# Performance work log

Measured on AMD Instinct MI355X. Metric: run time of the kernel, lower is better.

The kernel has to match this reference:

```python
import jax, jax.numpy as jnp
from jax import lax
import numpy as np

SHAPE = (50, 60, 65)   # -> after net: (17, 27, 32), flatten = 14688
NEG = 0.01             # LeakyReLU default slope
B, N = 8, 80000        # batch size, total active voxels


def _lrelu(x):
    return jnp.where(x >= 0, x, NEG * x)


def _sparse_conv(x, w, b, m):
    # Regular (non-submanifold) sparse conv == dense VALID conv on densified
    # input (inactive sites are 0 so they contribute nothing). Output site is
    # active iff any input site in the kernel footprint is active; bias is
    # added only at active output sites.
    k = w.shape[2]
    y = lax.conv_general_dilated(x, w, (1, 1, 1), 'VALID',
                                 dimension_numbers=('NCDHW', 'OIDHW', 'NCDHW'))
    m2 = lax.reduce_window(m, 0.0, lax.max, (1, 1, k, k, k), (1, 1, 1, 1, 1), 'VALID')
    y = jnp.where(m2 > 0, y + b[None, :, None, None, None], 0.0)
    return y, m2


def _sparse_maxpool(x, m, k):
    # spconv SparseMaxPool: max over ACTIVE sites only (inactive excluded, not 0)
    xm = jnp.where(m > 0, x, -jnp.inf)
    p = lax.reduce_window(xm, -jnp.inf, lax.max, (1, 1, k, k, k), (1, 1, 1, 1, 1), 'VALID')
    m2 = lax.reduce_window(m, 0.0, lax.max, (1, 1, k, k, k), (1, 1, 1, 1, 1), 'VALID')
    return jnp.where(m2 > 0, p, 0.0), m2


def setup_inputs() -> dict:
    key = jax.random.key(0)
    ks = jax.random.split(key, 24)
    D, H, W = SHAPE
    features = jax.random.normal(ks[0], (N, 1), dtype=jnp.float32)
    bi = jax.random.randint(ks[1], (N,), 0, B)
    zi = jax.random.randint(ks[2], (N,), 0, D)
    yi = jax.random.randint(ks[3], (N,), 0, H)
    xi = jax.random.randint(ks[4], (N,), 0, W)
    coors = jnp.stack([bi, zi, yi, xi], axis=1).astype(jnp.int32)
    s = 0.05
    p = {}
    p['w1'] = jax.random.normal(ks[5], (32, 1, 4, 4, 4), jnp.float32) * s
    p['b1'] = jax.random.normal(ks[6], (32,), jnp.float32) * s
    p['w2'] = jax.random.normal(ks[7], (32, 32, 4, 4, 4), jnp.float32) * s
    p['b2'] = jax.random.normal(ks[8], (32,), jnp.float32) * s
    p['w3'] = jax.random.normal(ks[9], (32, 32, 4, 4, 4), jnp.float32) * s
    p['b3'] = jax.random.normal(ks[10], (32,), jnp.float32) * s
    p['w4'] = jax.random.normal(ks[11], (32, 32, 4, 4, 4), jnp.float32) * s
    p['b4'] = jax.random.normal(ks[12], (32,), jnp.float32) * s
    p['w5'] = jax.random.normal(ks[13], (32, 32, 4, 4, 4), jnp.float32) * s
    p['b5'] = jax.random.normal(ks[14], (32,), jnp.float32) * s
    p['w6'] = jax.random.normal(ks[15], (32, 32, 4, 4, 4), jnp.float32) * s
    p['b6'] = jax.random.normal(ks[16], (32,), jnp.float32) * s
    p['w7'] = jax.random.normal(ks[17], (1, 32, 4, 4, 4), jnp.float32) * s
    p['b7'] = jax.random.normal(ks[18], (1,), jnp.float32) * s
    p['W8'] = jax.random.normal(ks[19], (14688, 1000), jnp.float32) * 0.01
    p['b8'] = jax.random.normal(ks[20], (1000,), jnp.float32) * s
    p['W9'] = jax.random.normal(ks[21], (1000, 1000), jnp.float32) * 0.03
    p['b9'] = jax.random.normal(ks[22], (1000,), jnp.float32) * s
    p['W10'] = jax.random.normal(ks[23], (1000, 1), jnp.float32) * 0.03
    p['b10'] = jnp.zeros((1,), jnp.float32)
    return dict(features=features, coors=coors, batch_size=B, **p)


def reference(features, coors, batch_size,
              w1, b1, w2, b2, w3, b3, w4, b4, w5, b5, w6, b6, w7, b7,
              W8, b8, W9, b9, W10, b10):
    D, H, W = SHAPE
    bi, zi, yi, xi = coors[:, 0], coors[:, 1], coors[:, 2], coors[:, 3]
    dense = jnp.zeros((batch_size, 1, D, H, W), features.dtype)
    dense = dense.at[bi, 0, zi, yi, xi].set(features[:, 0])
    mask = jnp.zeros((batch_size, 1, D, H, W), features.dtype)
    mask = mask.at[bi, 0, zi, yi, xi].set(1.0)

    x, m = _sparse_conv(dense, w1, b1, mask); x = _lrelu(x)
    x, m = _sparse_conv(x, w2, b2, m);        x = _lrelu(x)
    x, m = _sparse_maxpool(x, m, 5)
    x, m = _sparse_conv(x, w3, b3, m);        x = _lrelu(x)
    x, m = _sparse_conv(x, w4, b4, m);        x = _lrelu(x)
    x, m = _sparse_maxpool(x, m, 5)
    x, m = _sparse_conv(x, w5, b5, m);        x = _lrelu(x)
    x, m = _sparse_conv(x, w6, b6, m);        x = _lrelu(x)
    x, m = _sparse_conv(x, w7, b7, m);        x = _lrelu(x)
    x, m = _sparse_maxpool(x, m, 5)

    # ToDense (inactive sites already 0) + Flatten -> [B, 14688]
    h = x.reshape(x.shape[0], -1)
    h = _lrelu(h @ W8 + b8)
    h = _lrelu(h @ W9 + b9)
    out = _lrelu(h @ W10 + b10)
    return out
```

## Files before the change

### kernel.cpp

```cpp
#include <hip/hip_runtime.h>
#include <cstddef>


#define NEGSLOPE 0.01f
#define NINF (-3.0e38f)

#define TZ 4
#define TY 4
#define TXT 16
#define IZ 7
#define IY 7
#define IX 19
#define NV (IZ*IY*IX)

typedef __attribute__((ext_vector_type(8)))  short    short8;
typedef __attribute__((ext_vector_type(4)))  unsigned uint4v;
typedef __attribute__((ext_vector_type(16))) float    floatx16;

constexpr int ilog2c(int v) { return v == 1 ? 0 : 1 + ilog2c(v / 2); }

__device__ __forceinline__ float lrelu(float v) { return v >= 0.f ? v : NEGSLOPE * v; }

__device__ __forceinline__ unsigned short f2bf(float f) {
  unsigned b = __float_as_uint(f);
  return (unsigned short)((b + 0x7fffu + ((b >> 16) & 1u)) >> 16);
}
__device__ __forceinline__ float bf2f(unsigned short h) {
  return __uint_as_float(((unsigned)h) << 16);
}
__device__ __forceinline__ unsigned splitpair(float a, float b, unsigned& lo) {
  unsigned short ha = f2bf(a), hb = f2bf(b);
  unsigned short la = f2bf(a - bf2f(ha)), lb = f2bf(b - bf2f(hb));
  lo = (unsigned)la | ((unsigned)lb << 16);
  return (unsigned)ha | ((unsigned)hb << 16);
}

__device__ __forceinline__ short8 ld_frag(const uint2* s2, int v, int oct) {
  uint2 u0 = s2[v * 5 + oct * 2];
  uint2 u1 = s2[v * 5 + oct * 2 + 1];
  uint4v t; t.x = u0.x; t.y = u0.y; t.z = u1.x; t.w = u1.y;
  return __builtin_bit_cast(short8, t);
}

__global__ void k_claim(const int* __restrict__ coors, unsigned* __restrict__ claim, int N) {
  int i = blockIdx.x * blockDim.x + threadIdx.x;
  if (i >= N) return;
  int b = coors[4*i], z = coors[4*i+1], y = coors[4*i+2], x = coors[4*i+3];
  int v = ((b*50 + z)*60 + y)*65 + x;
  atomicMax(&claim[v], (unsigned)(i + 1));
}

__global__ void k_scatter(const int* __restrict__ coors, const float* __restrict__ feat,
                          const unsigned* __restrict__ claim,
                          float* __restrict__ x0, float* __restrict__ m0, int N) {
  int i = blockIdx.x * blockDim.x + threadIdx.x;
  if (i >= N) return;
  int b = coors[4*i], z = coors[4*i+1], y = coors[4*i+2], x = coors[4*i+3];
  int v = ((b*50 + z)*60 + y)*65 + x;
  m0[v] = 1.f;
  if (claim[v] == (unsigned)(i + 1)) x0[v] = feat[i];
}

__global__ void k_repack(const float* __restrict__ w, float* __restrict__ wr, int CI, int CO) {
  int i = blockIdx.x * blockDim.x + threadIdx.x;
  int tot = CO * CI * 64;
  if (i >= tot) return;
  int k = i & 63;
  int ci = (i >> 6) % CI;
  int co = i / (64 * CI);
  wr[(k * CI + ci) * CO + co] = w[i];
}

__global__ void k_repack_mfma(const float* __restrict__ w, unsigned short* __restrict__ tbl) {
  int i = blockIdx.x * blockDim.x + threadIdx.x;
  if (i >= 64*4*2*64) return;
  int lane = i & 63; int t = i >> 6;
  int pack = t & 1; t >>= 1;
  int pass = t & 3; int tap = t >> 2;
  int co = lane & 31; int oct = lane >> 5;
#pragma unroll
  for (int j = 0; j < 8; ++j) {
    int k = oct * 8 + j;
    int ci = pass * 8 + (k & 7);
    int part = ((k >> 3) ^ pack) & 1;
    float wv = w[((co * 32 + ci) << 6) + tap];
    unsigned short wh = f2bf(wv);
    unsigned short r = part ? f2bf(wv - bf2f(wh)) : wh;
    tbl[(size_t)i * 8 + j] = r;
  }
}

__global__ void kd_z(const float* __restrict__ in, float* __restrict__ o,
                     int Zi, int Yi, int Xi, int Zo, int K, int nI) {
  int gid = blockIdx.x * blockDim.x + threadIdx.x;
  int perOut = Zo * Yi * Xi;
  if (gid >= nI * perOut) return;
  int item = gid / perOut;
  int r = gid - item * perOut;
  int x = r % Xi; int t = r / Xi;
  int y = t % Yi; int z = t / Yi;
  const float* ib = in + (size_t)item * Zi * Yi * Xi;
  float mx = 0.f;
  for (int d = 0; d < K; d++) mx = fmaxf(mx, ib[((z + d) * Yi + y) * Xi + x]);
  o[gid] = mx;
}

__global__ void kd_y(const float* __restrict__ in, float* __restrict__ o,
                     int Zo, int Yi, int Xi, int Yo, int K, int nI) {
  int gid = blockIdx.x * blockDim.x + threadIdx.x;
  int perOut = Zo * Yo * Xi;
  if (gid >= nI * perOut) return;
  int item = gid / perOut;
  int r = gid - item * perOut;
  int x = r % Xi; int t = r / Xi;
  int y = t % Yo; int z = t / Yo;
  const float* ib = in + (size_t)item * Zo * Yi * Xi;
  float mx = 0.f;
  for (int d = 0; d < K; d++) mx = fmaxf(mx, ib[(z * Yi + y + d) * Xi + x]);
  o[gid] = mx;
}

__global__ void kd_x(const float* __restrict__ in, float* __restrict__ o,
                     int Zo, int Yo, int Xi, int Xo, int K, int nI) {
  int gid = blockIdx.x * blockDim.x + threadIdx.x;
  int perOut = Zo * Yo * Xo;
  if (gid >= nI * perOut) return;
  int item = gid / perOut;
  int r = gid - item * perOut;
  int x = r % Xo; int t = r / Xo;
  int y = t % Yo; int z = t / Yo;
  const float* ib = in + (size_t)item * Zo * Yo * Xi;
  float mx = 0.f;
  for (int d = 0; d < K; d++) mx = fmaxf(mx, ib[(z * Yo + y) * Xi + x + d]);
  o[gid] = mx;
}

template<int TZL, int TYL, int TXL, int IZL, int IYL, int IXL>
__global__ __launch_bounds__(256, 4)
void k_conv32m(const float* __restrict__ in, const unsigned short* __restrict__ tbl,
               const float* __restrict__ bias, const float* __restrict__ mo,
               float* __restrict__ out,
               int Zi, int Yi, int Xi, int Zo, int Yo, int Xo,
               int tilesZ, int tilesY, int tilesX) {
  constexpr int NVL = IZL * IYL * IXL;
  constexpr int LXs = ilog2c(TXL);
  constexpr int LYs = ilog2c(TYL);
  __shared__ unsigned sU[NVL * 10];
  const int perIn = Zi * Yi * Xi;
  const int perOut = Zo * Yo * Xo;
  int bid = blockIdx.x;
  int txi = bid % tilesX; bid /= tilesX;
  int tyi = bid % tilesY; bid /= tilesY;
  int tzi = bid % tilesZ; int item = bid / tilesZ;
  const int z0 = tzi * TZL, y0 = tyi * TYL, x0 = txi * TXL;
  const int tid = threadIdx.x;
  const int lane = tid & 63;
  const int col = lane & 31;
  const int oct = lane >> 5;
  const int wv  = tid >> 6;

  int lvBase0, lvBase1;
  {
    int vt0 = (2*wv + 0)*32 + col;
    int vt1 = (2*wv + 1)*32 + col;
    lvBase0 = ((vt0 >> (LXs+LYs))*IYL + ((vt0 >> LXs) & (TYL-1)))*IXL + (vt0 & (TXL-1));
    lvBase1 = ((vt1 >> (LXs+LYs))*IYL + ((vt1 >> LXs) & (TYL-1)))*IXL + (vt1 & (TXL-1));
  }

  floatx16 acc0, acc1;
#pragma unroll
  for (int r = 0; r < 16; ++r) { acc0[r] = 0.f; acc1[r] = 0.f; }

  const float* inb = in + (size_t)item * perIn * 32;
  const char* tb = (const char*)tbl + lane * 16;
  uint2* s2 = (uint2*)sU;

#pragma unroll 1
  for (int p = 0; p < 4; ++p) {
    __syncthreads();
    for (int idx = tid; idx < NVL; idx += 256) {
      int iz = idx / (IYL * IXL); int r = idx - iz * (IYL * IXL);
      int iy = r / IXL; int ix = r - iy * IXL;
      int gz = z0 + iz, gy = y0 + iy, gx = x0 + ix;
      float4 f0 = make_float4(0.f,0.f,0.f,0.f), f1 = make_float4(0.f,0.f,0.f,0.f);
      if (gz < Zi && gy < Yi && gx < Xi) {
        const float* vp = inb + (size_t)((gz * Yi + gy) * Xi + gx) * 32 + p * 8;
        f0 = *(const float4*)vp;
        f1 = *(const float4*)(vp + 4);
      }
      unsigned l0, l1, l2, l3;
      unsigned h0 = splitpair(f0.x, f0.y, l0);
      unsigned h1 = splitpair(f0.z, f0.w, l1);
      unsigned h2 = splitpair(f1.x, f1.y, l2);
      unsigned h3 = splitpair(f1.z, f1.w, l3);
      s2[idx * 5 + 0] = make_uint2(h0, h1);
      s2[idx * 5 + 1] = make_uint2(h2, h3);
      s2[idx * 5 + 2] = make_uint2(l0, l1);
      s2[idx * 5 + 3] = make_uint2(l2, l3);
    }
    __syncthreads();

    const char* tp = tb + (size_t)p * 2048;
#pragma unroll 2
    for (int tap = 0; tap < 64; ++tap) {
      int kz = tap >> 4, ky = (tap >> 2) & 3, kx = tap & 3;
      int sOff = (kz * IYL + ky) * IXL + kx;
      short8 b0 = *(const short8*)(tp + (size_t)tap * 8192);
      short8 b1 = *(const short8*)(tp + (size_t)tap * 8192 + 1024);
      short8 a0 = ld_frag(s2, lvBase0 + sOff, oct);
      short8 a1 = ld_frag(s2, lvBase1 + sOff, oct);
      acc0 = __builtin_amdgcn_mfma_f32_32x32x16_bf16(a0, b0, acc0, 0, 0, 0);
      acc0 = __builtin_amdgcn_mfma_f32_32x32x16_bf16(a0, b1, acc0, 0, 0, 0);
      acc1 = __builtin_amdgcn_mfma_f32_32x32x16_bf16(a1, b0, acc1, 0, 0, 0);
      acc1 = __builtin_amdgcn_mfma_f32_32x32x16_bf16(a1, b1, acc1, 0, 0, 0);
    }
  }

  const float bco = bias[col];
#pragma unroll
  for (int gg = 0; gg < 2; ++gg) {
    int vtb = (2*wv + gg) * 32;
#pragma unroll
    for (int rg = 0; rg < 16; ++rg) {
      int row = (rg & 3) + 8 * (rg >> 2) + 4 * oct;
      int vt = vtb + row;
      int oz = vt >> (LXs+LYs), oy = (vt >> LXs) & (TYL-1), ox = vt & (TXL-1);
      int gz = z0 + oz, gy = y0 + oy, gx = x0 + ox;
      if (gz < Zo && gy < Yo && gx < Xo) {
        int ov = item * perOut + (gz * Yo + gy) * Xo + gx;
        float val = (gg == 0) ? acc0[rg] : acc1[rg];
        bool act = mo[ov] > 0.f;
        out[(size_t)ov * 32 + col] = lrelu(act ? (val + bco) : 0.f);
      }
    }
  }
}

template<int TZL, int TYL, int TXL, int IZL, int IYL, int IXL>
static void launch_conv32(hipStream_t stream,
                          const float* in, const unsigned short* tbl, const float* bias,
                          const float* mo, float* o,
                          int Zi, int Yi, int Xi, int Zo, int Yo, int Xo, int nI) {
  int tz = (Zo + TZL - 1) / TZL, ty = (Yo + TYL - 1) / TYL, tx = (Xo + TXL - 1) / TXL;
  k_conv32m<TZL,TYL,TXL,IZL,IYL,IXL><<<nI * tz * ty * tx, 256, 0, stream>>>(
      in, tbl, bias, mo, o, Zi, Yi, Xi, Zo, Yo, Xo, tz, ty, tx);
}

__global__ __launch_bounds__(256, 2)
void k_conv1t(const float* __restrict__ in, const float* __restrict__ wr,
              const float* __restrict__ bias, const float* __restrict__ mo,
              float* __restrict__ out,
              int Zi, int Yi, int Xi, int Zo, int Yo, int Xo,
              int tilesZ, int tilesY, int tilesX) {
  __shared__ float sinf[NV];
  __shared__ float4 wsh[512];
  {
    const float4* wr4 = (const float4*)wr;
    for (int idx = threadIdx.x; idx < 512; idx += 256) wsh[idx] = wr4[idx];
  }
  const int perIn = Zi * Yi * Xi;
  const int perOut = Zo * Yo * Xo;
  int bid = blockIdx.x;
  int txi = bid % tilesX; bid /= tilesX;
  int tyi = bid % tilesY; bid /= tilesY;
  int tzi = bid % tilesZ; int item = bid / tilesZ;
  const int z0 = tzi * TZ, y0 = tyi * TY, x0 = txi * TXT;
  const int tid = threadIdx.x;
  const int ox = tid & 15, oy = (tid >> 4) & 3, oz = tid >> 6;

  const float* inb = in + (size_t)item * perIn;
  for (int idx = tid; idx < NV; idx += 256) {
    int iz = idx / (IY * IX); int r = idx - iz * (IY * IX);
    int iy = r / IX; int ix = r - iy * IX;
    int gz = z0 + iz, gy = y0 + iy, gx = x0 + ix;
    float val = 0.f;
    if (gz < Zi && gy < Yi && gx < Xi)
      val = inb[(size_t)((gz * Yi + gy) * Xi + gx)];
    sinf[idx] = val;
  }
  __syncthreads();

  float4 acc[8];
#pragma unroll
  for (int j = 0; j < 8; ++j) acc[j] = make_float4(0.f, 0.f, 0.f, 0.f);

#pragma unroll 1
  for (int tap = 0; tap < 64; ++tap) {
    int kz = tap >> 4, ky = (tap >> 2) & 3, kx = tap & 3;
    int lv = ((oz + kz) * IY + (oy + ky)) * IX + (ox + kx);
    float av = sinf[lv];
#pragma unroll
    for (int j = 0; j < 8; ++j) {
      float4 wvv = wsh[tap * 8 + j];
      acc[j].x = fmaf(av, wvv.x, acc[j].x);
      acc[j].y = fmaf(av, wvv.y, acc[j].y);
      acc[j].z = fmaf(av, wvv.z, acc[j].z);
      acc[j].w = fmaf(av, wvv.w, acc[j].w);
    }
  }

  int gz = z0 + oz, gy = y0 + oy, gx = x0 + ox;
  if (gz < Zo && gy < Yo && gx < Xo) {
    int ov = item * perOut + (gz * Yo + gy) * Xo + gx;
    bool act = mo[ov] > 0.f;
    const float4* b4 = (const float4*)bias;
    float* op = out + (size_t)ov * 32;
#pragma unroll
    for (int j = 0; j < 8; ++j) {
      float4 r = acc[j]; float4 bj = b4[j];
      r.x = lrelu(act ? (r.x + bj.x) : 0.f);
      r.y = lrelu(act ? (r.y + bj.y) : 0.f);
      r.z = lrelu(act ? (r.z + bj.z) : 0.f);
      r.w = lrelu(act ? (r.w + bj.w) : 0.f);
      *(float4*)(op + j * 4) = r;
    }
  }
}

__global__ __launch_bounds__(256, 2)
void k_conv7t(const float* __restrict__ in, const float* __restrict__ wr,
              const float* __restrict__ bias, const float* __restrict__ mo,
              float* __restrict__ out,
              int Zi, int Yi, int Xi, int Zo, int Yo, int Xo,
              int tilesZ, int tilesY, int tilesX) {
  __shared__ float4 sin4[4][NV];
  __shared__ float4 wsh[512];
  {
    const float4* wr4 = (const float4*)wr;
    for (int idx = threadIdx.x; idx < 512; idx += 256) wsh[idx] = wr4[idx];
  }
  const int perIn = Zi * Yi * Xi;
  const int perOut = Zo * Yo * Xo;
  int bid = blockIdx.x;
  int txi = bid % tilesX; bid /= tilesX;
  int tyi = bid % tilesY; bid /= tilesY;
  int tzi = bid % tilesZ; int item = bid / tilesZ;
  const int z0 = tzi * TZ, y0 = tyi * TY, x0 = txi * TXT;
  const int tid = threadIdx.x;
  const int ox = tid & 15, oy = (tid >> 4) & 3, oz = tid >> 6;

  const float* inb = in + (size_t)item * perIn * 32;
  float acc = 0.f;

#pragma unroll 1
  for (int h = 0; h < 2; ++h) {
    __syncthreads();
    for (int idx = tid; idx < NV * 4; idx += 256) {
      int q = idx / NV; int v = idx - q * NV;
      int iz = v / (IY * IX); int r = v - iz * (IY * IX);
      int iy = r / IX; int ix = r - iy * IX;
      int gz = z0 + iz, gy = y0 + iy, gx = x0 + ix;
      float4 val = make_float4(0.f, 0.f, 0.f, 0.f);
      if (gz < Zi && gy < Yi && gx < Xi)
        val = *(const float4*)(inb + (size_t)((gz * Yi + gy) * Xi + gx) * 32 + h * 16 + q * 4);
      sin4[q][v] = val;
    }
    __syncthreads();
#pragma unroll 1
    for (int tap = 0; tap < 64; ++tap) {
      int kz = tap >> 4, ky = (tap >> 2) & 3, kx = tap & 3;
      int lv = ((oz + kz) * IY + (oy + ky)) * IX + (ox + kx);
      float4 a0 = sin4[0][lv];
      float4 a1 = sin4[1][lv];
      float4 a2 = sin4[2][lv];
      float4 a3 = sin4[3][lv];
      float4 w0 = wsh[tap * 8 + h * 4 + 0];
      float4 w1 = wsh[tap * 8 + h * 4 + 1];
      float4 w2 = wsh[tap * 8 + h * 4 + 2];
      float4 w3 = wsh[tap * 8 + h * 4 + 3];
      acc += a0.x*w0.x + a0.y*w0.y + a0.z*w0.z + a0.w*w0.w
           + a1.x*w1.x + a1.y*w1.y + a1.z*w1.z + a1.w*w1.w
           + a2.x*w2.x + a2.y*w2.y + a2.z*w2.z + a2.w*w2.w
           + a3.x*w3.x + a3.y*w3.y + a3.z*w3.z + a3.w*w3.w;
    }
  }

  int gz = z0 + oz, gy = y0 + oy, gx = x0 + ox;
  if (gz < Zo && gy < Yo && gx < Xo) {
    int ov = item * perOut + (gz * Yo + gy) * Xo + gx;
    bool act = mo[ov] > 0.f;
    out[ov] = lrelu(act ? (acc + bias[0]) : 0.f);
  }
}

__global__ void k_pool_z(const float* __restrict__ in, const float* __restrict__ m,
                         float* __restrict__ out, int Zi, int Yi, int Xi, int Zo, int nI) {
  int gid = blockIdx.x * blockDim.x + threadIdx.x;
  int perOut = Zo * Yi * Xi;
  int tot = nI * perOut * 8;
  if (gid >= tot) return;
  int c4 = gid & 7; int v = gid >> 3;
  int item = v / perOut;
  int r = v - item * perOut;
  int x = r % Xi; int t = r / Xi;
  int y = t % Yi; int z = t / Yi;
  int ib = item * Zi * Yi * Xi;
  float4 acc = {NINF, NINF, NINF, NINF};
  for (int j = 0; j < 5; j++) {
    int vi = ib + ((z + j)*Yi + y)*Xi + x;
    if (m[vi] > 0.f) {
      float4 val = *(const float4*)(in + (size_t)vi*32 + c4*4);
      acc.x = fmaxf(acc.x, val.x); acc.y = fmaxf(acc.y, val.y);
      acc.z = fmaxf(acc.z, val.z); acc.w = fmaxf(acc.w, val.w);
    }
  }
  *(float4*)(out + (size_t)v*32 + c4*4) = acc;
}

__global__ void k_pool_y(const float* __restrict__ in, float* __restrict__ out,
                         int Z, int Yi, int Xi, int Yo, int nI) {
  int gid = blockIdx.x * blockDim.x + threadIdx.x;
  int perOut = Z * Yo * Xi;
  int tot = nI * perOut * 8;
  if (gid >= tot) return;
  int c4 = gid & 7; int v = gid >> 3;
  int item = v / perOut;
  int r = v - item * perOut;
  int x = r % Xi; int t = r / Xi;
  int y = t % Yo; int z = t / Yo;
  int ib = item * Z * Yi * Xi;
  float4 acc = {NINF, NINF, NINF, NINF};
  for (int j = 0; j < 5; j++) {
    int vi = ib + (z*Yi + y + j)*Xi + x;
    float4 val = *(const float4*)(in + (size_t)vi*32 + c4*4);
    acc.x = fmaxf(acc.x, val.x); acc.y = fmaxf(acc.y, val.y);
    acc.z = fmaxf(acc.z, val.z); acc.w = fmaxf(acc.w, val.w);
  }
  *(float4*)(out + (size_t)v*32 + c4*4) = acc;
}

__global__ void k_pool_x(const float* __restrict__ in, const float* __restrict__ mp,
                         float* __restrict__ out, int Z, int Y, int Xi, int Xo, int nI) {
  int gid = blockIdx.x * blockDim.x + threadIdx.x;
  int perOut = Z * Y * Xo;
  int tot = nI * perOut * 8;
  if (gid >= tot) return;
  int c4 = gid & 7; int v = gid >> 3;
  int item = v / perOut;
  int r = v - item * perOut;
  int x = r % Xo; int t = r / Xo;
  int y = t % Y; int z = t / Y;
  int ib = item * Z * Y * Xi;
  float4 acc = {NINF, NINF, NINF, NINF};
  for (int j = 0; j < 5; j++) {
    int vi = ib + (z*Y + y)*Xi + x + j;
    float4 val = *(const float4*)(in + (size_t)vi*32 + c4*4);
    acc.x = fmaxf(acc.x, val.x); acc.y = fmaxf(acc.y, val.y);
    acc.z = fmaxf(acc.z, val.z); acc.w = fmaxf(acc.w, val.w);
  }
  bool act = mp[v] > 0.f;
  float4 rr;
  rr.x = act ? acc.x : 0.f; rr.y = act ? acc.y : 0.f;
  rr.z = act ? acc.z : 0.f; rr.w = act ? acc.w : 0.f;
  *(float4*)(out + (size_t)v*32 + c4*4) = rr;
}

__global__ void k_pool3(const float* __restrict__ xin, const float* __restrict__ m,
                        const float* __restrict__ mp, float* __restrict__ out, int nI) {
  int gid = blockIdx.x * blockDim.x + threadIdx.x;
  int perOut = 17 * 27 * 32;
  int tot = nI * perOut;
  if (gid >= tot) return;
  int item = gid / perOut;
  int r = gid - item * perOut;
  int x = r & 31; int t = r >> 5;
  int y = t % 27; int z = t / 27;
  const float* xb = xin + (size_t)item * 23436;
  const float* mb = m + (size_t)item * 23436;
  float acc = NINF;
  for (int dz = 0; dz < 5; dz++)
    for (int dy = 0; dy < 5; dy++) {
      const float* rowx = xb + (size_t)(((z + dz)*31 + y + dy)*36 + x);
      const float* rowm = mb + (size_t)(((z + dz)*31 + y + dy)*36 + x);
      for (int dx = 0; dx < 5; dx++)
        if (rowm[dx] > 0.f) acc = fmaxf(acc, rowx[dx]);
    }
  out[gid] = (mp[gid] > 0.f) ? acc : 0.f;
}

__global__ __launch_bounds__(256, 4)
void k_fc_part(const float* __restrict__ X, const float* __restrict__ Wm,
               float* __restrict__ part, int K, int Ncol, int Kc) {
  __shared__ float sm[16][16][8];
  int ks = blockIdx.y;
  int k0 = ks * Kc;
  int k1 = k0 + Kc; if (k1 > K) k1 = K;
  int cl = threadIdx.x & 15;
  int kt = threadIdx.x >> 4;
  int col = blockIdx.x * 16 + cl;
  float a0=0.f,a1=0.f,a2=0.f,a3=0.f,a4=0.f,a5=0.f,a6=0.f,a7=0.f;
  if (col < Ncol) {
    for (int k = k0 + kt; k < k1; k += 16) {
      float w = Wm[(size_t)k * Ncol + col];
      a0 += X[0 * K + k] * w; a1 += X[1 * K + k] * w;
      a2 += X[2 * K + k] * w; a3 += X[3 * K + k] * w;
      a4 += X[4 * K + k] * w; a5 += X[5 * K + k] * w;
      a6 += X[6 * K + k] * w; a7 += X[7 * K + k] * w;
    }
  }
  sm[kt][cl][0]=a0; sm[kt][cl][1]=a1; sm[kt][cl][2]=a2; sm[kt][cl][3]=a3;
  sm[kt][cl][4]=a4; sm[kt][cl][5]=a5; sm[kt][cl][6]=a6; sm[kt][cl][7]=a7;
  __syncthreads();
  if (threadIdx.x < 128) {
    int c = threadIdx.x & 15;
    int b = threadIdx.x >> 4;
    float s = 0.f;
#pragma unroll
    for (int k = 0; k < 16; k++) s += sm[k][c][b];
    int cc = blockIdx.x * 16 + c;
    if (cc < Ncol) part[((size_t)ks * 8 + b) * Ncol + cc] = s;
  }
}

__global__ void k_fc_fin(const float* __restrict__ part, int ns,
                         const float* __restrict__ bias, float* __restrict__ out, int Ncol) {
  int i = blockIdx.x * blockDim.x + threadIdx.x;
  if (i >= 8 * Ncol) return;
  int b = i / Ncol;
  int c = i - b * Ncol;
  float s = 0.f;
  for (int ks = 0; ks < ns; ks++) s += part[((size_t)ks * 8 + b) * Ncol + c];
  out[i] = lrelu(s + bias[c]);
}

__global__ __launch_bounds__(256, 4)
void k_fc(const float* __restrict__ X, const float* __restrict__ Wm,
          const float* __restrict__ bias, float* __restrict__ out,
          int K, int Ncol) {
  __shared__ float sm[16][16][8];
  int cl = threadIdx.x & 15;
  int kt = threadIdx.x >> 4;
  int col = blockIdx.x * 16 + cl;
  float a0=0.f,a1=0.f,a2=0.f,a3=0.f,a4=0.f,a5=0.f,a6=0.f,a7=0.f;
  if (col < Ncol) {
    for (int k = kt; k < K; k += 16) {
      float w = Wm[(size_t)k * Ncol + col];
      a0 += X[0 * K + k] * w; a1 += X[1 * K + k] * w;
      a2 += X[2 * K + k] * w; a3 += X[3 * K + k] * w;
      a4 += X[4 * K + k] * w; a5 += X[5 * K + k] * w;
      a6 += X[6 * K + k] * w; a7 += X[7 * K + k] * w;
    }
  }
  sm[kt][cl][0]=a0; sm[kt][cl][1]=a1; sm[kt][cl][2]=a2; sm[kt][cl][3]=a3;
  sm[kt][cl][4]=a4; sm[kt][cl][5]=a5; sm[kt][cl][6]=a6; sm[kt][cl][7]=a7;
  __syncthreads();
  if (threadIdx.x < 128) {
    int c = threadIdx.x & 15;
    int b = threadIdx.x >> 4;
    float s = 0.f;
#pragma unroll
    for (int k = 0; k < 16; k++) s += sm[k][c][b];
    int cc = blockIdx.x * 16 + c;
    if (cc < Ncol) out[b * Ncol + cc] = lrelu(s + bias[cc]);
  }
}

static inline int G256(long long n) { return (int)((n + 255) / 256); }

extern "C" void kernel_launch(void* const* d_in, const int* in_sizes, int n_in,
                              void* d_out, int out_size, void* d_ws, size_t ws_size,
                              hipStream_t stream) {
  const float* feat  = (const float*)d_in[0];
  const int*   coors = (const int*)d_in[1];
  const float* w1 = (const float*)d_in[3];  const float* b1 = (const float*)d_in[4];
  const float* w2 = (const float*)d_in[5];  const float* b2 = (const float*)d_in[6];
  const float* w3 = (const float*)d_in[7];  const float* b3 = (const float*)d_in[8];
  const float* w4 = (const float*)d_in[9];  const float* b4 = (const float*)d_in[10];
  const float* w5 = (const float*)d_in[11]; const float* b5 = (const float*)d_in[12];
  const float* w6 = (const float*)d_in[13]; const float* b6 = (const float*)d_in[14];
  const float* w7 = (const float*)d_in[15]; const float* b7 = (const float*)d_in[16];
  const float* W8 = (const float*)d_in[17]; const float* b8 = (const float*)d_in[18];
  const float* W9 = (const float*)d_in[19]; const float* b9 = (const float*)d_in[20];
  const float* W10= (const float*)d_in[21]; const float* b10= (const float*)d_in[22];
  float* out = (float*)d_out;

  char* ws = (char*)d_ws;
  size_t off = 0;
  auto alloc = [&](size_t nfloats) -> float* {
    float* p = (float*)(ws + off);
    off += ((nfloats * 4 + 1023) / 1024) * 1024;
    return p;
  };

  float* x0  = alloc(1560000);
  float* m0  = alloc(1560000);
  float* m1  = alloc(8 * 166098);
  float* m2  = alloc(8 * 140184);
  float* mp1 = alloc(8 * 110000);
  float* m3  = alloc(8 * 90428);
  float* m4  = alloc(8 * 73304);
  float* mp2 = alloc(8 * 54000);
  float* m5  = alloc(8 * 41958);
  float* m6  = alloc(8 * 31824);
  float* m7  = alloc(8 * 23436);
  float* mp3 = alloc(8 * 14688);
  float* p3  = alloc(8 * 14688);
  float* dt1 = alloc(8 * 183300);
  float* dt2 = alloc(8 * 174135);
  float* wr1 = alloc(2048);
  float* wr7 = alloc(2048);
  unsigned short* tb2 = (unsigned short*)alloc(131072);
  unsigned short* tb3 = (unsigned short*)alloc(131072);
  unsigned short* tb4 = (unsigned short*)alloc(131072);
  unsigned short* tb5 = (unsigned short*)alloc(131072);
  unsigned short* tb6 = (unsigned short*)alloc(131072);
  float* part= alloc(64000);
  float* h8  = alloc(8000);
  float* h9  = alloc(8000);
  size_t fixedOff = off;

  const size_t perItemAB = ((size_t)5315136*4 + 1023)/1024*1024
                         + ((size_t)4485888*4 + 1023)/1024*1024
                         + ((size_t)23436*4 + 1023)/1024*1024;
  int G = 0;
  for (int g : {8, 4, 2, 1})
    if (fixedOff + (size_t)g * perItemAB <= ws_size) { G = g; break; }
  if (G == 0) return;

  float* A  = alloc((size_t)G * 5315136);
  float* Bb = alloc((size_t)G * 4485888);
  float* x7 = alloc((size_t)G * 23436);
  unsigned* claim = (unsigned*)A;

  hipMemsetAsync(claim, 0, 1560000 * 4, stream);
  hipMemsetAsync(x0,    0, 1560000 * 4, stream);
  hipMemsetAsync(m0,    0, 1560000 * 4, stream);

  k_repack<<<G256(32*1*64),  256, 0, stream>>>(w1, wr1, 1, 32);
  k_repack<<<G256(1*32*64),  256, 0, stream>>>(w7, wr7, 32, 1);
  k_repack_mfma<<<128, 256, 0, stream>>>(w2, tb2);
  k_repack_mfma<<<128, 256, 0, stream>>>(w3, tb3);
  k_repack_mfma<<<128, 256, 0, stream>>>(w4, tb4);
  k_repack_mfma<<<128, 256, 0, stream>>>(w5, tb5);
  k_repack_mfma<<<128, 256, 0, stream>>>(w6, tb6);

  const int N = 80000;
  k_claim  <<<G256(N), 256, 0, stream>>>(coors, claim, N);
  k_scatter<<<G256(N), 256, 0, stream>>>(coors, feat, claim, x0, m0, N);

  auto dil3 = [&](const float* src, float* dst,
                  int Zi, int Yi, int Xi, int Zo, int Yo, int Xo, int K) {
    kd_z<<<G256((long long)8*Zo*Yi*Xi), 256, 0, stream>>>(src, dt1, Zi,Yi,Xi, Zo, K, 8);
    kd_y<<<G256((long long)8*Zo*Yo*Xi), 256, 0, stream>>>(dt1, dt2, Zo,Yi,Xi, Yo, K, 8);
    kd_x<<<G256((long long)8*Zo*Yo*Xo), 256, 0, stream>>>(dt2, dst, Zo,Yo,Xi, Xo, K, 8);
  };
  dil3(m0,  m1,  50,60,65, 47,57,62, 4);
  dil3(m1,  m2,  47,57,62, 44,54,59, 4);
  dil3(m2,  mp1, 44,54,59, 40,50,55, 5);
  dil3(mp1, m3,  40,50,55, 37,47,52, 4);
  dil3(m3,  m4,  37,47,52, 34,44,49, 4);
  dil3(m4,  mp2, 34,44,49, 30,40,45, 5);
  dil3(mp2, m5,  30,40,45, 27,37,42, 4);
  dil3(m5,  m6,  27,37,42, 24,34,39, 4);
  dil3(m6,  m7,  24,34,39, 21,31,36, 4);
  dil3(m7,  mp3, 21,31,36, 17,27,32, 5);

  for (int g0 = 0; g0 < 8; g0 += G) {
    const float* x0g  = x0  + (size_t)g0 * 195000;
    const float* m1g  = m1  + (size_t)g0 * 166098;
    const float* m2g  = m2  + (size_t)g0 * 140184;
    const float* mp1g = mp1 + (size_t)g0 * 110000;
    const float* m3g  = m3  + (size_t)g0 * 90428;
    const float* m4g  = m4  + (size_t)g0 * 73304;
    const float* mp2g = mp2 + (size_t)g0 * 54000;
    const float* m5g  = m5  + (size_t)g0 * 41958;
    const float* m6g  = m6  + (size_t)g0 * 31824;
    const float* m7g  = m7  + (size_t)g0 * 23436;
    const float* mp3g = mp3 + (size_t)g0 * 14688;

    {
      int tz = (47 + TZ - 1) / TZ, ty = (57 + TY - 1) / TY, tx = (62 + TXT - 1) / TXT;
      k_conv1t<<<G * tz * ty * tx, 256, 0, stream>>>(
          x0g, wr1, b1, m1g, A, 50,60,65, 47,57,62, tz, ty, tx);
    }
    launch_conv32<4,4,16,7,7,19>(stream, A, tb2, b2, m2g, Bb, 47,57,62, 44,54,59, G);
    k_pool_z<<<G256((long long)G*127440*8), 256, 0, stream>>>(Bb, m2g,  A,  44,54,59, 40, G);
    k_pool_y<<<G256((long long)G*118000*8), 256, 0, stream>>>(A,  Bb, 40,54,59, 50, G);
    k_pool_x<<<G256((long long)G*110000*8), 256, 0, stream>>>(Bb, mp1g, A,  40,50,59, 55, G);
    launch_conv32<8,8,4,11,11,7>(stream, A, tb3, b3, m3g, Bb, 40,50,55, 37,47,52, G);
    launch_conv32<4,16,4,7,19,7>(stream, Bb, tb4, b4, m4g, A, 37,47,52, 34,44,49, G);
    k_pool_z<<<G256((long long)G*64680*8), 256, 0, stream>>>(A,  m4g,  Bb, 34,44,49, 30, G);
    k_pool_y<<<G256((long long)G*58800*8), 256, 0, stream>>>(Bb, A,  30,44,49, 40, G);
    k_pool_x<<<G256((long long)G*54000*8), 256, 0, stream>>>(A,  mp2g, Bb, 30,40,49, 45, G);
    launch_conv32<4,4,16,7,7,19>(stream, Bb, tb5, b5, m5g, A, 30,40,45, 27,37,42, G);
    launch_conv32<8,4,8,11,7,11>(stream, A, tb6, b6, m6g, Bb, 27,37,42, 24,34,39, G);
    {
      int tz = (21 + TZ - 1) / TZ, ty = (31 + TY - 1) / TY, tx = (36 + TXT - 1) / TXT;
      k_conv7t<<<G * tz * ty * tx, 256, 0, stream>>>(
          Bb, wr7, b7, m7g, x7, 24,34,39, 21,31,36, tz, ty, tx);
    }
    k_pool3<<<G256((long long)G*14688), 256, 0, stream>>>(
        x7, m7g, mp3g, p3 + (size_t)g0 * 14688, G);
  }

  k_fc_part<<<dim3(63, 8), 256, 0, stream>>>(p3, W8, part, 14688, 1000, 1836);
  k_fc_fin <<<G256(8000), 256, 0, stream>>>(part, 8, b8, h8, 1000);
  k_fc_part<<<dim3(63, 4), 256, 0, stream>>>(h8, W9, part, 1000, 1000, 250);
  k_fc_fin <<<G256(8000), 256, 0, stream>>>(part, 4, b9, h9, 1000);
  k_fc<<<1, 256, 0, stream>>>(h9, W10, b10, out, 1000, 1);
}
```

Baseline: 3.301 ms.

## Write -inf at inactive conv outputs to drop mask reads, fuse pool y/x passes

Convolutions whose outputs feed a max-pool now write -inf at inactive sites. The pool kernels can then take a plain max without reading the input mask, and the extra mask loads and branches go away. The separate y and x pooling passes are merged into one kernel in which each thread handles four x outputs from a shared 8-wide window. This removes one launch and one full intermediate round-trip per pooling stage, at the cost of more registers per thread and a dependence on -inf sentinels being handled correctly downstream.

```diff
diff --git a/kernel.cpp b/kernel.cpp
--- a/kernel.cpp
+++ b/kernel.cpp
@@ -135,7 +135,7 @@
   o[gid] = mx;
 }
 
-template<int TZL, int TYL, int TXL, int IZL, int IYL, int IXL>
+template<int TZL, int TYL, int TXL, int IZL, int IYL, int IXL, bool POOLOUT>
 __global__ __launch_bounds__(256, 4)
 void k_conv32m(const float* __restrict__ in, const unsigned short* __restrict__ tbl,
                const float* __restrict__ bias, const float* __restrict__ mo,
@@ -230,19 +230,20 @@
         int ov = item * perOut + (gz * Yo + gy) * Xo + gx;
         float val = (gg == 0) ? acc0[rg] : acc1[rg];
         bool act = mo[ov] > 0.f;
-        out[(size_t)ov * 32 + col] = lrelu(act ? (val + bco) : 0.f);
+        float vv = act ? lrelu(val + bco) : (POOLOUT ? NINF : 0.f);
+        out[(size_t)ov * 32 + col] = vv;
       }
     }
   }
 }
 
-template<int TZL, int TYL, int TXL, int IZL, int IYL, int IXL>
+template<int TZL, int TYL, int TXL, int IZL, int IYL, int IXL, bool POOLOUT>
 static void launch_conv32(hipStream_t stream,
                           const float* in, const unsigned short* tbl, const float* bias,
                           const float* mo, float* o,
                           int Zi, int Yi, int Xi, int Zo, int Yo, int Xo, int nI) {
   int tz = (Zo + TZL - 1) / TZL, ty = (Yo + TYL - 1) / TYL, tx = (Xo + TXL - 1) / TXL;
-  k_conv32m<TZL,TYL,TXL,IZL,IYL,IXL><<<nI * tz * ty * tx, 256, 0, stream>>>(
+  k_conv32m<TZL,TYL,TXL,IZL,IYL,IXL,POOLOUT><<<nI * tz * ty * tx, 256, 0, stream>>>(
       in, tbl, bias, mo, o, Zi, Yi, Xi, Zo, Yo, Xo, tz, ty, tx);
 }
 
@@ -379,12 +380,12 @@
   if (gz < Zo && gy < Yo && gx < Xo) {
     int ov = item * perOut + (gz * Yo + gy) * Xo + gx;
     bool act = mo[ov] > 0.f;
-    out[ov] = lrelu(act ? (acc + bias[0]) : 0.f);
-  }
-}
-
-__global__ void k_pool_z(const float* __restrict__ in, const float* __restrict__ m,
-                         float* __restrict__ out, int Zi, int Yi, int Xi, int Zo, int nI) {
+    out[ov] = act ? lrelu(acc + bias[0]) : NINF;
+  }
+}
+
+__global__ void k_pool_z(const float* __restrict__ in, float* __restrict__ out,
+                         int Zi, int Yi, int Xi, int Zo, int nI) {
   int gid = blockIdx.x * blockDim.x + threadIdx.x;
   int perOut = Zo * Yi * Xi;
   int tot = nI * perOut * 8;
@@ -398,30 +399,6 @@
   float4 acc = {NINF, NINF, NINF, NINF};
   for (int j = 0; j < 5; j++) {
     int vi = ib + ((z + j)*Yi + y)*Xi + x;
-    if (m[vi] > 0.f) {
-      float4 val = *(const float4*)(in + (size_t)vi*32 + c4*4);
-      acc.x = fmaxf(acc.x, val.x); acc.y = fmaxf(acc.y, val.y);
-      acc.z = fmaxf(acc.z, val.z); acc.w = fmaxf(acc.w, val.w);
-    }
-  }
-  *(float4*)(out + (size_t)v*32 + c4*4) = acc;
-}
-
-__global__ void k_pool_y(const float* __restrict__ in, float* __restrict__ out,
-                         int Z, int Yi, int Xi, int Yo, int nI) {
-  int gid = blockIdx.x * blockDim.x + threadIdx.x;
-  int perOut = Z * Yo * Xi;
-  int tot = nI * perOut * 8;
-  if (gid >= tot) return;
-  int c4 = gid & 7; int v = gid >> 3;
-  int item = v / perOut;
-  int r = v - item * perOut;
-  int x = r % Xi; int t = r / Xi;
-  int y = t % Yo; int z = t / Yo;
-  int ib = item * Z * Yi * Xi;
-  float4 acc = {NINF, NINF, NINF, NINF};
-  for (int j = 0; j < 5; j++) {
-    int vi = ib + (z*Yi + y + j)*Xi + x;
     float4 val = *(const float4*)(in + (size_t)vi*32 + c4*4);
     acc.x = fmaxf(acc.x, val.x); acc.y = fmaxf(acc.y, val.y);
     acc.z = fmaxf(acc.z, val.z); acc.w = fmaxf(acc.w, val.w);
@@ -429,33 +406,60 @@
   *(float4*)(out + (size_t)v*32 + c4*4) = acc;
 }
 
-__global__ void k_pool_x(const float* __restrict__ in, const float* __restrict__ mp,
-                         float* __restrict__ out, int Z, int Y, int Xi, int Xo, int nI) {
+__global__ void k_pool_yx(const float* __restrict__ in, const float* __restrict__ mp,
+                          float* __restrict__ out,
+                          int Z, int Yi, int Xi, int Yo, int Xo, int nI) {
   int gid = blockIdx.x * blockDim.x + threadIdx.x;
-  int perOut = Z * Y * Xo;
-  int tot = nI * perOut * 8;
+  int runsX = (Xo + 3) >> 2;
+  int perR = Z * Yo * runsX;
+  int tot = nI * perR * 8;
   if (gid >= tot) return;
-  int c4 = gid & 7; int v = gid >> 3;
-  int item = v / perOut;
-  int r = v - item * perOut;
-  int x = r % Xo; int t = r / Xo;
-  int y = t % Y; int z = t / Y;
-  int ib = item * Z * Y * Xi;
-  float4 acc = {NINF, NINF, NINF, NINF};
-  for (int j = 0; j < 5; j++) {
-    int vi = ib + (z*Y + y)*Xi + x + j;
-    float4 val = *(const float4*)(in + (size_t)vi*32 + c4*4);
-    acc.x = fmaxf(acc.x, val.x); acc.y = fmaxf(acc.y, val.y);
-    acc.z = fmaxf(acc.z, val.z); acc.w = fmaxf(acc.w, val.w);
-  }
-  bool act = mp[v] > 0.f;
-  float4 rr;
-  rr.x = act ? acc.x : 0.f; rr.y = act ? acc.y : 0.f;
-  rr.z = act ? acc.z : 0.f; rr.w = act ? acc.w : 0.f;
-  *(float4*)(out + (size_t)v*32 + c4*4) = rr;
-}
-
-__global__ void k_pool3(const float* __restrict__ xin, const float* __restrict__ m,
+  int c4 = gid & 7; int r = gid >> 3;
+  int item = r / perR;
+  int rr = r - item * perR;
+  int xr = rr % runsX; int t = rr / runsX;
+  int y = t % Yo; int z = t / Yo;
+  int x0 = xr << 2;
+  const float* ib = in + (size_t)item * Z * Yi * Xi * 32;
+
+  float4 ym[8];
+#pragma unroll
+  for (int dx = 0; dx < 8; ++dx) ym[dx] = make_float4(NINF, NINF, NINF, NINF);
+#pragma unroll
+  for (int dy = 0; dy < 5; ++dy) {
+    const float* rowb = ib + (size_t)((z * Yi + y + dy) * Xi) * 32;
+#pragma unroll
+    for (int dx = 0; dx < 8; ++dx) {
+      int xx = x0 + dx;
+      if (xx < Xi) {
+        float4 v = *(const float4*)(rowb + (size_t)xx * 32 + c4 * 4);
+        ym[dx].x = fmaxf(ym[dx].x, v.x); ym[dx].y = fmaxf(ym[dx].y, v.y);
+        ym[dx].z = fmaxf(ym[dx].z, v.z); ym[dx].w = fmaxf(ym[dx].w, v.w);
+      }
+    }
+  }
+  int perOut = Z * Yo * Xo;
+#pragma unroll
+  for (int j = 0; j < 4; ++j) {
+    int xx = x0 + j;
+    if (xx < Xo) {
+      float4 a = ym[j];
+#pragma unroll
+      for (int d = 1; d < 5; ++d) {
+        a.x = fmaxf(a.x, ym[j+d].x); a.y = fmaxf(a.y, ym[j+d].y);
+        a.z = fmaxf(a.z, ym[j+d].z); a.w = fmaxf(a.w, ym[j+d].w);
+      }
+      int v = item * perOut + (z * Yo + y) * Xo + xx;
+      bool act = mp[v] > 0.f;
+      float4 rrv;
+      rrv.x = act ? a.x : 0.f; rrv.y = act ? a.y : 0.f;
+      rrv.z = act ? a.z : 0.f; rrv.w = act ? a.w : 0.f;
+      *(float4*)(out + (size_t)v*32 + c4*4) = rrv;
+    }
+  }
+}
+
+__global__ void k_pool3(const float* __restrict__ xin,
                         const float* __restrict__ mp, float* __restrict__ out, int nI) {
   int gid = blockIdx.x * blockDim.x + threadIdx.x;
   int perOut = 17 * 27 * 32;
@@ -466,14 +470,12 @@
   int x = r & 31; int t = r >> 5;
   int y = t % 27; int z = t / 27;
   const float* xb = xin + (size_t)item * 23436;
-  const float* mb = m + (size_t)item * 23436;
   float acc = NINF;
   for (int dz = 0; dz < 5; dz++)
     for (int dy = 0; dy < 5; dy++) {
       const float* rowx = xb + (size_t)(((z + dz)*31 + y + dy)*36 + x);
-      const float* rowm = mb + (size_t)(((z + dz)*31 + y + dy)*36 + x);
       for (int dx = 0; dx < 5; dx++)
-        if (rowm[dx] > 0.f) acc = fmaxf(acc, rowx[dx]);
+        acc = fmaxf(acc, rowx[dx]);
     }
   out[gid] = (mp[gid] > 0.f) ? acc : 0.f;
 }
@@ -673,24 +675,22 @@
       k_conv1t<<<G * tz * ty * tx, 256, 0, stream>>>(
           x0g, wr1, b1, m1g, A, 50,60,65, 47,57,62, tz, ty, tx);
     }
-    launch_conv32<4,4,16,7,7,19>(stream, A, tb2, b2, m2g, Bb, 47,57,62, 44,54,59, G);
-    k_pool_z<<<G256((long long)G*127440*8), 256, 0, stream>>>(Bb, m2g,  A,  44,54,59, 40, G);
-    k_pool_y<<<G256((long long)G*118000*8), 256, 0, stream>>>(A,  Bb, 40,54,59, 50, G);
-    k_pool_x<<<G256((long long)G*110000*8), 256, 0, stream>>>(Bb, mp1g, A,  40,50,59, 55, G);
-    launch_conv32<8,8,4,11,11,7>(stream, A, tb3, b3, m3g, Bb, 40,50,55, 37,47,52, G);
-    launch_conv32<4,16,4,7,19,7>(stream, Bb, tb4, b4, m4g, A, 37,47,52, 34,44,49, G);
-    k_pool_z<<<G256((long long)G*64680*8), 256, 0, stream>>>(A,  m4g,  Bb, 34,44,49, 30, G);
-    k_pool_y<<<G256((long long)G*58800*8), 256, 0, stream>>>(Bb, A,  30,44,49, 40, G);
-    k_pool_x<<<G256((long long)G*54000*8), 256, 0, stream>>>(A,  mp2g, Bb, 30,40,49, 45, G);
-    launch_conv32<4,4,16,7,7,19>(stream, Bb, tb5, b5, m5g, A, 30,40,45, 27,37,42, G);
-    launch_conv32<8,4,8,11,7,11>(stream, A, tb6, b6, m6g, Bb, 27,37,42, 24,34,39, G);
+    launch_conv32<4,4,16,7,7,19,true>(stream, A, tb2, b2, m2g, Bb, 47,57,62, 44,54,59, G);
+    k_pool_z<<<G256((long long)G*127440*8), 256, 0, stream>>>(Bb, A, 44,54,59, 40, G);
+    k_pool_yx<<<G256((long long)G*40*50*14*8), 256, 0, stream>>>(A, mp1g, Bb, 40,54,59, 50,55, G);
+    launch_conv32<8,8,4,11,11,7,false>(stream, Bb, tb3, b3, m3g, A, 40,50,55, 37,47,52, G);
+    launch_conv32<4,16,4,7,19,7,true>(stream, A, tb4, b4, m4g, Bb, 37,47,52, 34,44,49, G);
+    k_pool_z<<<G256((long long)G*64680*8), 256, 0, stream>>>(Bb, A, 34,44,49, 30, G);
+    k_pool_yx<<<G256((long long)G*30*40*12*8), 256, 0, stream>>>(A, mp2g, Bb, 30,44,49, 40,45, G);
+    launch_conv32<4,4,16,7,7,19,false>(stream, Bb, tb5, b5, m5g, A, 30,40,45, 27,37,42, G);
+    launch_conv32<8,4,8,11,7,11,false>(stream, A, tb6, b6, m6g, Bb, 27,37,42, 24,34,39, G);
     {
       int tz = (21 + TZ - 1) / TZ, ty = (31 + TY - 1) / TY, tx = (36 + TXT - 1) / TXT;
       k_conv7t<<<G * tz * ty * tx, 256, 0, stream>>>(
           Bb, wr7, b7, m7g, x7, 24,34,39, 21,31,36, tz, ty, tx);
     }
     k_pool3<<<G256((long long)G*14688), 256, 0, stream>>>(
-        x7, m7g, mp3g, p3 + (size_t)g0 * 14688, G);
+        x7, mp3g, p3 + (size_t)g0 * 14688, G);
   }
 
   k_fc_part<<<dim3(63, 8), 256, 0, stream>>>(p3, W8, part, 14688, 1000, 1836);
```

New measurement: 3.198 ms. 3.1% less time.
